# Kernel optimization log

Measured on AMD Instinct MI355X. Metric: run time of the kernel, lower is better.

Reference implementation:

```python
import jax, jax.numpy as jnp
import numpy as np

DIM = 1024
DEPTH = 4
D_STATE = 16
D_CONV = 4
D_INNER = 2 * DIM
DT_RANK = (DIM + 15) // 16  # 64, ceil(dim/16) as in mamba-ssm
B_SZ, L = 4, 2048


def setup_inputs() -> dict:
    key = jax.random.key(0)
    ks = jax.random.split(key, 10)
    s = 0.02
    x = jax.random.normal(ks[0], (B_SZ, L, DIM), jnp.float32)
    in_proj_w = jax.random.normal(ks[1], (DEPTH, 2 * D_INNER, DIM), jnp.float32) * s
    conv_w = jax.random.normal(ks[2], (DEPTH, D_INNER, D_CONV), jnp.float32) * 0.2
    conv_b = jnp.zeros((DEPTH, D_INNER), jnp.float32)
    x_proj_w = jax.random.normal(ks[3], (DEPTH, DT_RANK + 2 * D_STATE, D_INNER), jnp.float32) * s
    dt_proj_w = jax.random.normal(ks[4], (DEPTH, D_INNER, DT_RANK), jnp.float32) * s
    # bias init so softplus(bias) ~ 0.01 (mamba dt_init)
    dt_proj_b = jnp.full((DEPTH, D_INNER), float(np.log(np.expm1(0.01))), jnp.float32)
    # S4D-real init: A = -(1..d_state)
    A_log = jnp.broadcast_to(jnp.log(jnp.arange(1, D_STATE + 1, dtype=jnp.float32)), (D_INNER, D_STATE))
    A_log = jnp.broadcast_to(A_log, (DEPTH, D_INNER, D_STATE))
    D = jnp.ones((DEPTH, D_INNER), jnp.float32)
    out_proj_w = jax.random.normal(ks[5], (DEPTH, DIM, D_INNER), jnp.float32) * s
    return {"x": x, "in_proj_w": in_proj_w, "conv_w": conv_w, "conv_b": conv_b,
            "x_proj_w": x_proj_w, "dt_proj_w": dt_proj_w, "dt_proj_b": dt_proj_b,
            "A_log": A_log, "D": D, "out_proj_w": out_proj_w}


def _selective_scan(u, delta, A, Bm, Cm, D):
    # u, delta: [B, L, d_inner]; Bm, Cm: [B, L, d_state]; A: [d_inner, d_state]
    def step(h, inp):
        u_t, d_t, b_t, c_t = inp  # [B,di], [B,di], [B,ds], [B,ds]
        dA = jnp.exp(d_t[:, :, None] * A)                 # [B,di,ds]
        h = dA * h + (d_t * u_t)[:, :, None] * b_t[:, None, :]
        y = jnp.einsum('bds,bs->bd', h, c_t)
        return h, y

    h0 = jnp.zeros((u.shape[0], u.shape[2], A.shape[1]), u.dtype)
    xs = (u.transpose(1, 0, 2), delta.transpose(1, 0, 2),
          Bm.transpose(1, 0, 2), Cm.transpose(1, 0, 2))
    _, ys = jax.lax.scan(step, h0, xs)                     # ys: [L,B,di]
    return ys.transpose(1, 0, 2) + u * D


def _mamba_layer(x, in_w, cw, cb, xp_w, dtw, dtb, A_log, D, ow):
    xz = jnp.einsum('bld,ed->ble', x, in_w)               # [B,L,2*di]
    xi, z = jnp.split(xz, 2, axis=-1)
    # causal depthwise conv over L
    xc = jax.lax.conv_general_dilated(
        xi.transpose(0, 2, 1),                             # [B,di,L]
        cw[:, None, :],                                    # [di,1,k]
        window_strides=(1,), padding=[(D_CONV - 1, 0)],
        feature_group_count=D_INNER,
        dimension_numbers=('NCH', 'OIH', 'NCH'))
    xc = jax.nn.silu(xc.transpose(0, 2, 1) + cb)           # [B,L,di]
    dbc = jnp.einsum('bld,ed->ble', xc, xp_w)              # [B,L,dt_rank+2*ds]
    dt, Bm, Cm = jnp.split(dbc, [DT_RANK, DT_RANK + D_STATE], axis=-1)
    delta = jax.nn.softplus(jnp.einsum('blr,dr->bld', dt, dtw) + dtb)
    A = -jnp.exp(A_log)
    y = _selective_scan(xc, delta, A, Bm, Cm, D)
    y = y * jax.nn.silu(z)
    return jnp.einsum('bld,od->blo', y, ow)


def reference(x, in_proj_w, conv_w, conv_b, x_proj_w, dt_proj_w, dt_proj_b, A_log, D, out_proj_w):
    for i in range(DEPTH):
        x = _mamba_layer(x, in_proj_w[i], conv_w[i], conv_b[i], x_proj_w[i],
                         dt_proj_w[i], dt_proj_b[i], A_log[i], D[i], out_proj_w[i])
    return x
```

## Files before the change

kernel.cpp:

```cpp
#include <hip/hip_runtime.h>
#include <hip/hip_bf16.h>
#include <math.h>

#define DIMK 1024
#define NDEPTH 4
#define DS 16
#define DCONV 4
#define DI 2048
#define DTR 64
#define NB 4
#define SL 2048
#define MT (NB * SL)
#define NXZ (2 * DI)
#define NDBC (DTR + 2 * DS)

typedef float f32x4 __attribute__((ext_vector_type(4)));
typedef short short8 __attribute__((ext_vector_type(8)));
typedef short short4v __attribute__((ext_vector_type(4)));

__device__ inline unsigned short f2bf(float f) {
    unsigned u = __builtin_bit_cast(unsigned, f);
    unsigned r = (u + 0x7FFFu + ((u >> 16) & 1u)) >> 16;
    return (unsigned short)r;
}
__device__ inline float bf2f(unsigned short h) {
    unsigned u = ((unsigned)h) << 16;
    return __builtin_bit_cast(float, u);
}
__device__ inline void split_bf(float f, unsigned short& hi, unsigned short& lo) {
    hi = f2bf(f);
    lo = f2bf(f - bf2f(hi));
}
__device__ inline unsigned short cvt1(float f) {
    __hip_bfloat16 t = __float2bfloat16(f);
    return __builtin_bit_cast(unsigned short, t);
}
__device__ inline void mfma16(f32x4& d, short8 a, short8 b) {
    asm volatile("v_mfma_f32_16x16x32_bf16 %0, %1, %2, %0"
                 : "+v"(d) : "v"(a), "v"(b));
}
__device__ __forceinline__ float dpp_sum16(float p) {
    asm("v_add_f32_dpp %0, %0, %0 quad_perm:[1,0,3,2] row_mask:0xf bank_mask:0xf bound_ctrl:0" : "+v"(p));
    asm("v_add_f32_dpp %0, %0, %0 quad_perm:[2,3,0,1] row_mask:0xf bank_mask:0xf bound_ctrl:0" : "+v"(p));
    asm("v_add_f32_dpp %0, %0, %0 row_ror:4 row_mask:0xf bank_mask:0xf bound_ctrl:0" : "+v"(p));
    asm("v_add_f32_dpp %0, %0, %0 row_ror:8 row_mask:0xf bank_mask:0xf bound_ctrl:0" : "+v"(p));
    return p;
}
__device__ __forceinline__ float exp2_raw(float x) {
    float r;
    asm("v_exp_f32 %0, %1" : "=v"(r) : "v"(x));
    return r;
}
__device__ __forceinline__ void gload16(const unsigned short* g, unsigned short* l) {
    __builtin_amdgcn_global_load_lds(
        (const __attribute__((address_space(1))) unsigned int*)(g),
        (__attribute__((address_space(3))) unsigned int*)(l),
        16, 0, 0);
}

__global__ __launch_bounds__(256) void cvt_bf16(
    const float* __restrict__ s, unsigned short* __restrict__ d, int n4)
{
    const int g = blockIdx.x * 256 + threadIdx.x;
    if (g < n4) {
        const float4 f = *(const float4*)(s + (size_t)g * 4);
        short4v v;
        v[0] = (short)cvt1(f.x); v[1] = (short)cvt1(f.y);
        v[2] = (short)cvt1(f.z); v[3] = (short)cvt1(f.w);
        *(short4v*)(d + (size_t)g * 4) = v;
    }
}

__global__ __launch_bounds__(256) void cvt_layer(
    const float* __restrict__ wi, const float* __restrict__ owp,
    const float* __restrict__ dtwp,
    unsigned short* __restrict__ wi16, unsigned short* __restrict__ ow16,
    unsigned short* __restrict__ dtwh, unsigned short* __restrict__ dtwl,
    int fastd)
{
    int g = blockIdx.x * 256 + threadIdx.x;
    const int n4w = NXZ * DIMK / 4;
    const int n4o = DIMK * DI / 4;
    const int n4d = DI * DTR / 4;
    if (g < n4w) {
        const float4 f = *(const float4*)(wi + (size_t)g * 4);
        short4v v;
        v[0] = (short)cvt1(f.x); v[1] = (short)cvt1(f.y);
        v[2] = (short)cvt1(f.z); v[3] = (short)cvt1(f.w);
        *(short4v*)(wi16 + (size_t)g * 4) = v;
        return;
    }
    g -= n4w;
    if (g < n4o) {
        const float4 f = *(const float4*)(owp + (size_t)g * 4);
        short4v v;
        v[0] = (short)cvt1(f.x); v[1] = (short)cvt1(f.y);
        v[2] = (short)cvt1(f.z); v[3] = (short)cvt1(f.w);
        *(short4v*)(ow16 + (size_t)g * 4) = v;
        return;
    }
    g -= n4o;
    if (g < n4d && fastd) {
        const float4 f = *(const float4*)(dtwp + (size_t)g * 4);
        short4v h4, l4;
        #pragma unroll
        for (int e = 0; e < 4; ++e) {
            unsigned short h, l;
            split_bf((&f.x)[e], h, l);
            h4[e] = (short)h; l4[e] = (short)l;
        }
        *(short4v*)(dtwh + (size_t)g * 4) = h4;
        *(short4v*)(dtwl + (size_t)g * 4) = l4;
    }
}

template <int CBF>
__global__ __launch_bounds__(256) void gemm_bb(
    const unsigned short* __restrict__ A, const unsigned short* __restrict__ B,
    void* __restrict__ Cv, int K, int lda, int ldb, int ldc)
{
    __shared__ unsigned short As[2][128 * 32];
    __shared__ unsigned short Bs[2][128 * 32];
    int id = blockIdx.y * gridDim.x + blockIdx.x;
    const int qq = (gridDim.x * gridDim.y) >> 3;
    id = (id & 7) * qq + (id >> 3);
    const int bm = (id / gridDim.x) * 128, bn = (id % gridDim.x) * 128;

    const int tid = threadIdx.x;
    const int wv = tid >> 6, ln = tid & 63;
    const int wr = wv >> 1, wc = wv & 1;
    const int fr = ln & 15, kg = ln >> 4;
    const int sr0 = wv * 32 + (ln >> 2);
    const int sr1 = sr0 + 16;
    const int sl = ln & 3;
    const int cg0 = sl ^ ((sr0 >> 1) & 3);
    const int cg1 = sl ^ ((sr1 >> 1) & 3);
    const unsigned short* pa0 = A + (size_t)(bm + sr0) * lda + cg0 * 8;
    const unsigned short* pa1 = A + (size_t)(bm + sr1) * lda + cg1 * 8;
    const unsigned short* pb0 = B + (size_t)(bn + sr0) * ldb + cg0 * 8;
    const unsigned short* pb1 = B + (size_t)(bn + sr1) * ldb + cg1 * 8;
    const int ldst0 = (wv * 32 + 0) * 32;
    const int ldst1 = (wv * 32 + 16) * 32;
    int offA[4], offB[4];
    #pragma unroll
    for (int f = 0; f < 4; ++f) {
        const int ra = wr * 64 + f * 16 + fr;
        offA[f] = ra * 32 + ((kg ^ ((ra >> 1) & 3)) * 8);
        const int rb = wc * 64 + f * 16 + fr;
        offB[f] = rb * 32 + ((kg ^ ((rb >> 1) & 3)) * 8);
    }
    f32x4 acc[4][4] = {};
    gload16(pa0, &As[0][ldst0]);
    gload16(pa1, &As[0][ldst1]);
    gload16(pb0, &Bs[0][ldst0]);
    gload16(pb1, &Bs[0][ldst1]);
    __syncthreads();
    int cur = 0;
    for (int k0 = 0; k0 < K; k0 += 32) {
        const int nxt = cur ^ 1;
        if (k0 + 32 < K) {
            gload16(pa0 + k0 + 32, &As[nxt][ldst0]);
            gload16(pa1 + k0 + 32, &As[nxt][ldst1]);
            gload16(pb0 + k0 + 32, &Bs[nxt][ldst0]);
            gload16(pb1 + k0 + 32, &Bs[nxt][ldst1]);
        }
        short8 af[4], bw[4];
        #pragma unroll
        for (int f = 0; f < 4; ++f) {
            af[f] = *(const short8*)&As[cur][offA[f]];
            bw[f] = *(const short8*)&Bs[cur][offB[f]];
        }
        #pragma unroll
        for (int fi = 0; fi < 4; ++fi)
            #pragma unroll
            for (int fj = 0; fj < 4; ++fj)
                mfma16(acc[fi][fj], af[fi], bw[fj]);
        __syncthreads();
        cur = nxt;
    }
    #pragma unroll
    for (int fi = 0; fi < 4; ++fi) {
        const int m0 = bm + wr * 64 + fi * 16 + kg * 4;
        #pragma unroll
        for (int fj = 0; fj < 4; ++fj) {
            const int n = bn + wc * 64 + fj * 16 + fr;
            #pragma unroll
            for (int q = 0; q < 4; ++q) {
                if (CBF) {
                    unsigned short* Cs = (unsigned short*)Cv;
                    Cs[(size_t)(m0 + q) * ldc + n] = cvt1(acc[fi][fj][q]);
                } else {
                    float* Cf = (float*)Cv;
                    Cf[(size_t)(m0 + q) * ldc + n] = acc[fi][fj][q];
                }
            }
        }
    }
}

template <int CBF>
__global__ __launch_bounds__(256) void gemm_fb(
    const float* __restrict__ A, const unsigned short* __restrict__ B,
    void* __restrict__ Cv, int K, int lda, int ldb, int ldc)
{
    __shared__ unsigned short As[2][128 * 32];
    __shared__ unsigned short Bs[2][128 * 32];
    int id = blockIdx.y * gridDim.x + blockIdx.x;
    const int qq = (gridDim.x * gridDim.y) >> 3;
    id = (id & 7) * qq + (id >> 3);
    const int bm = (id / gridDim.x) * 128, bn = (id % gridDim.x) * 128;

    const int tid = threadIdx.x;
    const int wv = tid >> 6, ln = tid & 63;
    const int wr = wv >> 1, wc = wv & 1;
    const int fr = ln & 15, kg = ln >> 4;
    const int r = tid >> 1, hf = tid & 1;
    const int sr0 = wv * 32 + (ln >> 2);
    const int sr1 = sr0 + 16;
    const int sl = ln & 3;
    const int cg0 = sl ^ ((sr0 >> 1) & 3);
    const int cg1 = sl ^ ((sr1 >> 1) & 3);
    const unsigned short* pb0 = B + (size_t)(bn + sr0) * ldb + cg0 * 8;
    const unsigned short* pb1 = B + (size_t)(bn + sr1) * ldb + cg1 * 8;
    const int ldst0 = (wv * 32 + 0) * 32;
    const int ldst1 = (wv * 32 + 16) * 32;
    const float* ga = A + (size_t)(bm + r) * lda + hf * 16;
    const int pk0 = (2 * hf + 0) ^ ((r >> 1) & 3);
    const int pk1 = (2 * hf + 1) ^ ((r >> 1) & 3);
    int offA[4], offB[4];
    #pragma unroll
    for (int f = 0; f < 4; ++f) {
        const int ra = wr * 64 + f * 16 + fr;
        offA[f] = ra * 32 + ((kg ^ ((ra >> 1) & 3)) * 8);
        const int rb = wc * 64 + f * 16 + fr;
        offB[f] = rb * 32 + ((kg ^ ((rb >> 1) & 3)) * 8);
    }
    f32x4 acc[4][4] = {};
    {
        float4 f0 = *(const float4*)(ga + 0);
        float4 f1 = *(const float4*)(ga + 4);
        float4 f2 = *(const float4*)(ga + 8);
        float4 f3 = *(const float4*)(ga + 12);
        short8 v;
        v[0] = (short)cvt1(f0.x); v[1] = (short)cvt1(f0.y);
        v[2] = (short)cvt1(f0.z); v[3] = (short)cvt1(f0.w);
        v[4] = (short)cvt1(f1.x); v[5] = (short)cvt1(f1.y);
        v[6] = (short)cvt1(f1.z); v[7] = (short)cvt1(f1.w);
        *(short8*)&As[0][r * 32 + pk0 * 8] = v;
        v[0] = (short)cvt1(f2.x); v[1] = (short)cvt1(f2.y);
        v[2] = (short)cvt1(f2.z); v[3] = (short)cvt1(f2.w);
        v[4] = (short)cvt1(f3.x); v[5] = (short)cvt1(f3.y);
        v[6] = (short)cvt1(f3.z); v[7] = (short)cvt1(f3.w);
        *(short8*)&As[0][r * 32 + pk1 * 8] = v;
        gload16(pb0, &Bs[0][ldst0]);
        gload16(pb1, &Bs[0][ldst1]);
    }
    __syncthreads();
    int cur = 0;
    for (int k0 = 0; k0 < K; k0 += 32) {
        const int nxt = cur ^ 1;
        const bool more = (k0 + 32 < K);
        float4 f0, f1, f2, f3;
        if (more) {
            gload16(pb0 + k0 + 32, &Bs[nxt][ldst0]);
            gload16(pb1 + k0 + 32, &Bs[nxt][ldst1]);
            f0 = *(const float4*)(ga + k0 + 32);
            f1 = *(const float4*)(ga + k0 + 36);
            f2 = *(const float4*)(ga + k0 + 40);
            f3 = *(const float4*)(ga + k0 + 44);
        }
        short8 af[4], bw[4];
        #pragma unroll
        for (int f = 0; f < 4; ++f) {
            af[f] = *(const short8*)&As[cur][offA[f]];
            bw[f] = *(const short8*)&Bs[cur][offB[f]];
        }
        #pragma unroll
        for (int fi = 0; fi < 4; ++fi)
            #pragma unroll
            for (int fj = 0; fj < 4; ++fj)
                mfma16(acc[fi][fj], af[fi], bw[fj]);
        if (more) {
            short8 v;
            v[0] = (short)cvt1(f0.x); v[1] = (short)cvt1(f0.y);
            v[2] = (short)cvt1(f0.z); v[3] = (short)cvt1(f0.w);
            v[4] = (short)cvt1(f1.x); v[5] = (short)cvt1(f1.y);
            v[6] = (short)cvt1(f1.z); v[7] = (short)cvt1(f1.w);
            *(short8*)&As[nxt][r * 32 + pk0 * 8] = v;
            v[0] = (short)cvt1(f2.x); v[1] = (short)cvt1(f2.y);
            v[2] = (short)cvt1(f2.z); v[3] = (short)cvt1(f2.w);
            v[4] = (short)cvt1(f3.x); v[5] = (short)cvt1(f3.y);
            v[6] = (short)cvt1(f3.z); v[7] = (short)cvt1(f3.w);
            *(short8*)&As[nxt][r * 32 + pk1 * 8] = v;
        }
        __syncthreads();
        cur = nxt;
    }
    #pragma unroll
    for (int fi = 0; fi < 4; ++fi) {
        const int m0 = bm + wr * 64 + fi * 16 + kg * 4;
        #pragma unroll
        for (int fj = 0; fj < 4; ++fj) {
            const int n = bn + wc * 64 + fj * 16 + fr;
            #pragma unroll
            for (int q = 0; q < 4; ++q) {
                if (CBF) {
                    unsigned short* Cs = (unsigned short*)Cv;
                    Cs[(size_t)(m0 + q) * ldc + n] = cvt1(acc[fi][fj][q]);
                } else {
                    float* Cf = (float*)Cv;
                    Cf[(size_t)(m0 + q) * ldc + n] = acc[fi][fj][q];
                }
            }
        }
    }
}

__global__ __launch_bounds__(256) void gemm_mfma(
    const float* __restrict__ A, const float* __restrict__ W,
    float* __restrict__ C, int K, int lda, int ldc)
{
    __shared__ unsigned short As[128 * 32];
    __shared__ unsigned short Ws[128 * 32];
    const int tid = threadIdx.x;
    const int bm = blockIdx.y * 128;
    const int bn = blockIdx.x * 128;
    const int r = tid >> 1;
    const int h = tid & 1;
    const int wv = tid >> 6;
    const int wr = wv >> 1;
    const int wc = wv & 1;
    const int ln = tid & 63;
    const int fr = ln & 15;
    const int kg = ln >> 4;
    f32x4 acc[4][4] = {};
    const float* ga = A + (size_t)(bm + r) * lda + h * 16;
    const float* gw = W + (size_t)(bn + r) * K + h * 16;
    for (int k0 = 0; k0 < K; k0 += 32) {
        #pragma unroll
        for (int p = 0; p < 2; ++p) {
            const int pk = (2 * h + p) ^ ((r >> 1) & 3);
            float4 f0 = *(const float4*)(ga + k0 + p * 8);
            float4 f1 = *(const float4*)(ga + k0 + p * 8 + 4);
            short8 v;
            v[0] = (short)cvt1(f0.x); v[1] = (short)cvt1(f0.y);
            v[2] = (short)cvt1(f0.z); v[3] = (short)cvt1(f0.w);
            v[4] = (short)cvt1(f1.x); v[5] = (short)cvt1(f1.y);
            v[6] = (short)cvt1(f1.z); v[7] = (short)cvt1(f1.w);
            *(short8*)&As[r * 32 + pk * 8] = v;
            f0 = *(const float4*)(gw + k0 + p * 8);
            f1 = *(const float4*)(gw + k0 + p * 8 + 4);
            v[0] = (short)cvt1(f0.x); v[1] = (short)cvt1(f0.y);
            v[2] = (short)cvt1(f0.z); v[3] = (short)cvt1(f0.w);
            v[4] = (short)cvt1(f1.x); v[5] = (short)cvt1(f1.y);
            v[6] = (short)cvt1(f1.z); v[7] = (short)cvt1(f1.w);
            *(short8*)&Ws[r * 32 + pk * 8] = v;
        }
        __syncthreads();
        short8 af[4], bw[4];
        #pragma unroll
        for (int f = 0; f < 4; ++f) {
            const int ra = wr * 64 + f * 16 + fr;
            af[f] = *(const short8*)&As[ra * 32 + ((kg ^ ((ra >> 1) & 3)) * 8)];
            const int rb = wc * 64 + f * 16 + fr;
            bw[f] = *(const short8*)&Ws[rb * 32 + ((kg ^ ((rb >> 1) & 3)) * 8)];
        }
        #pragma unroll
        for (int fi = 0; fi < 4; ++fi)
            #pragma unroll
            for (int fj = 0; fj < 4; ++fj)
                mfma16(acc[fi][fj], af[fi], bw[fj]);
        __syncthreads();
    }
    #pragma unroll
    for (int fi = 0; fi < 4; ++fi) {
        const int m0 = bm + wr * 64 + fi * 16 + kg * 4;
        #pragma unroll
        for (int fj = 0; fj < 4; ++fj) {
            const int n = bn + wc * 64 + fj * 16 + fr;
            #pragma unroll
            for (int q = 0; q < 4; ++q)
                C[(size_t)(m0 + q) * ldc + n] = acc[fi][fj][q];
        }
    }
}

template <int WRDT>
__global__ __launch_bounds__(256) void gemm_xproj(
    const float* __restrict__ A, const float* __restrict__ W,
    float* __restrict__ C, int K, int lda,
    unsigned short* __restrict__ dth, unsigned short* __restrict__ dtl)
{
    __shared__ unsigned short Ah[128 * 32], Al[128 * 32];
    __shared__ unsigned short Wh[32 * 32], Wl[32 * 32];
    const int tid = threadIdx.x;
    const int bm = blockIdx.y * 128;
    const int bn = blockIdx.x * 32;
    const int r = tid >> 1, hf = tid & 1;
    const int wv = tid >> 6;
    const int ln = tid & 63, fr = ln & 15, kg = ln >> 4;
    const int wsr = tid >> 3;
    const int wc4 = (tid & 7) << 2;
    f32x4 acc[2][2] = {};
    const float* ga = A + (size_t)(bm + r) * lda + hf * 16;
    const float* gw = W + (size_t)(bn + wsr) * K + wc4;
    for (int k0 = 0; k0 < K; k0 += 32) {
        #pragma unroll
        for (int j = 0; j < 4; ++j) {
            const int col = hf * 16 + j * 4;
            const int ad = r * 32 + (((col >> 3) ^ ((r >> 1) & 3)) << 3) + (col & 7);
            const float4 fa = *(const float4*)(ga + k0 + j * 4);
            short4v h4, l4;
            #pragma unroll
            for (int e = 0; e < 4; ++e) {
                unsigned short hh, llo;
                split_bf((&fa.x)[e], hh, llo);
                h4[e] = (short)hh; l4[e] = (short)llo;
            }
            *(short4v*)&Ah[ad] = h4;
            *(short4v*)&Al[ad] = l4;
        }
        {
            const int ad = wsr * 32 + (((wc4 >> 3) ^ ((wsr >> 1) & 3)) << 3) + (wc4 & 7);
            const float4 fw = *(const float4*)(gw + k0);
            short4v h4, l4;
            #pragma unroll
            for (int e = 0; e < 4; ++e) {
                unsigned short hh, llo;
                split_bf((&fw.x)[e], hh, llo);
                h4[e] = (short)hh; l4[e] = (short)llo;
            }
            *(short4v*)&Wh[ad] = h4;
            *(short4v*)&Wl[ad] = l4;
        }
        __syncthreads();
        short8 ah[2], alo[2], bh[2], bl[2];
        #pragma unroll
        for (int f = 0; f < 2; ++f) {
            const int ra = wv * 32 + f * 16 + fr;
            const int ao = ra * 32 + ((kg ^ ((ra >> 1) & 3)) * 8);
            ah[f]  = *(const short8*)&Ah[ao];
            alo[f] = *(const short8*)&Al[ao];
            const int rb = f * 16 + fr;
            const int bo = rb * 32 + ((kg ^ ((rb >> 1) & 3)) * 8);
            bh[f] = *(const short8*)&Wh[bo];
            bl[f] = *(const short8*)&Wl[bo];
        }
        #pragma unroll
        for (int fi = 0; fi < 2; ++fi)
            #pragma unroll
            for (int fj = 0; fj < 2; ++fj) {
                mfma16(acc[fi][fj], ah[fi], bh[fj]);
                mfma16(acc[fi][fj], ah[fi], bl[fj]);
                mfma16(acc[fi][fj], alo[fi], bh[fj]);
            }
        __syncthreads();
    }
    #pragma unroll
    for (int fi = 0; fi < 2; ++fi) {
        const int m0 = bm + wv * 32 + fi * 16 + kg * 4;
        #pragma unroll
        for (int fj = 0; fj < 2; ++fj) {
            const int n = bn + fj * 16 + fr;
            #pragma unroll
            for (int q = 0; q < 4; ++q) {
                const float v = acc[fi][fj][q];
                C[(size_t)(m0 + q) * NDBC + n] = v;
                if (WRDT && n < DTR) {
                    unsigned short hh, llo;
                    split_bf(v, hh, llo);
                    dth[(size_t)(m0 + q) * DTR + n] = hh;
                    dtl[(size_t)(m0 + q) * DTR + n] = llo;
                }
            }
        }
    }
}

__global__ __launch_bounds__(256) void gemm_delta(
    const float* __restrict__ A, const float* __restrict__ W,
    float* __restrict__ C, const float* __restrict__ bias)
{
    __shared__ unsigned short Ah[128 * 32], Al[128 * 32];
    __shared__ unsigned short Wh[128 * 32], Wl[128 * 32];
    const int tid = threadIdx.x;
    const int bm = blockIdx.y * 128;
    const int bn = blockIdx.x * 128;
    const int r = tid >> 1, hf = tid & 1;
    const int wv = tid >> 6, wr = wv >> 1, wc = wv & 1;
    const int ln = tid & 63, fr = ln & 15, kg = ln >> 4;
    f32x4 acc[4][4] = {};
    const float* ga = A + (size_t)(bm + r) * NDBC + hf * 16;
    const float* gw = W + (size_t)(bn + r) * DTR + hf * 16;
    for (int k0 = 0; k0 < DTR; k0 += 32) {
        #pragma unroll
        for (int j = 0; j < 4; ++j) {
            const int col = hf * 16 + j * 4;
            const int ad = r * 32 + (((col >> 3) ^ ((r >> 1) & 3)) << 3) + (col & 7);
            const float4 fa = *(const float4*)(ga + k0 + j * 4);
            const float4 fw = *(const float4*)(gw + k0 + j * 4);
            short4v ah4, al4, wh4, wl4;
            #pragma unroll
            for (int e = 0; e < 4; ++e) {
                unsigned short hh, llo;
                split_bf((&fa.x)[e], hh, llo);
                ah4[e] = (short)hh; al4[e] = (short)llo;
                split_bf((&fw.x)[e], hh, llo);
                wh4[e] = (short)hh; wl4[e] = (short)llo;
            }
            *(short4v*)&Ah[ad] = ah4; *(short4v*)&Al[ad] = al4;
            *(short4v*)&Wh[ad] = wh4; *(short4v*)&Wl[ad] = wl4;
        }
        __syncthreads();
        short8 ah[4], alo[4], bh[4], bl[4];
        #pragma unroll
        for (int f = 0; f < 4; ++f) {
            const int ra = wr * 64 + f * 16 + fr;
            const int ao = ra * 32 + ((kg ^ ((ra >> 1) & 3)) * 8);
            ah[f]  = *(const short8*)&Ah[ao];
            alo[f] = *(const short8*)&Al[ao];
            const int rb = wc * 64 + f * 16 + fr;
            const int bo = rb * 32 + ((kg ^ ((rb >> 1) & 3)) * 8);
            bh[f] = *(const short8*)&Wh[bo];
            bl[f] = *(const short8*)&Wl[bo];
        }
        #pragma unroll
        for (int fi = 0; fi < 4; ++fi)
            #pragma unroll
            for (int fj = 0; fj < 4; ++fj) {
                mfma16(acc[fi][fj], ah[fi], bh[fj]);
                mfma16(acc[fi][fj], ah[fi], bl[fj]);
                mfma16(acc[fi][fj], alo[fi], bh[fj]);
            }
        __syncthreads();
    }
    #pragma unroll
    for (int fi = 0; fi < 4; ++fi) {
        const int m0 = bm + wr * 64 + fi * 16 + kg * 4;
        #pragma unroll
        for (int fj = 0; fj < 4; ++fj) {
            const int n = bn + wc * 64 + fj * 16 + fr;
            const float bb = bias[n];
            #pragma unroll
            for (int q = 0; q < 4; ++q) {
                float v = acc[fi][fj][q] + bb;
                v = (v > 20.f) ? v : log1pf(__expf(v));
                C[(size_t)(m0 + q) * NXZ + n] = v;
            }
        }
    }
}

__global__ __launch_bounds__(256) void gemm_delta_pre(
    const unsigned short* __restrict__ Ahg, const unsigned short* __restrict__ Alg,
    const unsigned short* __restrict__ Whg, const unsigned short* __restrict__ Wlg,
    float* __restrict__ C, const float* __restrict__ bias)
{
    __shared__ unsigned short sAh[128 * 64], sAl[128 * 64];
    __shared__ unsigned short sWh[128 * 64], sWl[128 * 64];
    const int tid = threadIdx.x;
    const int bm = blockIdx.y * 128;
    const int bn = blockIdx.x * 128;
    const int wv = tid >> 6, ln = tid & 63;
    const int wr = wv >> 1, wc = wv & 1;
    const int fr = ln & 15, kg = ln >> 4;
    const int srow = ln >> 3;
    const int g = ln & 7;
    const int half = g >> 2, sub = g & 3;
    #pragma unroll
    for (int j = 0; j < 4; ++j) {
        const int row = wv * 32 + j * 8 + srow;
        const int sub2 = sub ^ ((row >> 1) & 3);
        const int scol = half * 32 + sub2 * 8;
        const int dst = (wv * 32 + j * 8) * 64;
        gload16(Ahg + (size_t)(bm + row) * DTR + scol, sAh + dst);
        gload16(Alg + (size_t)(bm + row) * DTR + scol, sAl + dst);
        gload16(Whg + (size_t)(bn + row) * DTR + scol, sWh + dst);
        gload16(Wlg + (size_t)(bn + row) * DTR + scol, sWl + dst);
    }
    __syncthreads();
    f32x4 acc[4][4] = {};
    #pragma unroll
    for (int ks = 0; ks < 2; ++ks) {
        short8 ah[4], alo[4], bh[4], bl[4];
        #pragma unroll
        for (int f = 0; f < 4; ++f) {
            const int ra = wr * 64 + f * 16 + fr;
            const int ao = ra * 64 + ks * 32 + ((kg ^ ((ra >> 1) & 3)) * 8);
            ah[f]  = *(const short8*)&sAh[ao];
            alo[f] = *(const short8*)&sAl[ao];
            const int rb = wc * 64 + f * 16 + fr;
            const int bo = rb * 64 + ks * 32 + ((kg ^ ((rb >> 1) & 3)) * 8);
            bh[f] = *(const short8*)&sWh[bo];
            bl[f] = *(const short8*)&sWl[bo];
        }
        #pragma unroll
        for (int fi = 0; fi < 4; ++fi)
            #pragma unroll
            for (int fj = 0; fj < 4; ++fj) {
                mfma16(acc[fi][fj], ah[fi], bh[fj]);
                mfma16(acc[fi][fj], ah[fi], bl[fj]);
                mfma16(acc[fi][fj], alo[fi], bh[fj]);
            }
    }
    #pragma unroll
    for (int fi = 0; fi < 4; ++fi) {
        const int m0 = bm + wr * 64 + fi * 16 + kg * 4;
        #pragma unroll
        for (int fj = 0; fj < 4; ++fj) {
            const int n = bn + wc * 64 + fj * 16 + fr;
            const float bb = bias[n];
            #pragma unroll
            for (int q = 0; q < 4; ++q) {
                float v = acc[fi][fj][q] + bb;
                v = (v > 20.f) ? v : log1pf(__expf(v));
                C[(size_t)(m0 + q) * NXZ + n] = v;
            }
        }
    }
}

__global__ __launch_bounds__(256) void conv_silu(
    const float* __restrict__ xz, const float* __restrict__ cw,
    const float* __restrict__ cb, float* __restrict__ xc)
{
    const int g = blockIdx.x * 256 + threadIdx.x;
    const int c4 = g & (DI / 4 - 1);
    const int mq = g >> 9;
    const int m0 = mq << 2;
    const int l0 = m0 & (SL - 1);
    const int c = c4 << 2;
    const float4 w0 = *(const float4*)(cw + (size_t)(c + 0) * DCONV);
    const float4 w1 = *(const float4*)(cw + (size_t)(c + 1) * DCONV);
    const float4 w2 = *(const float4*)(cw + (size_t)(c + 2) * DCONV);
    const float4 w3 = *(const float4*)(cw + (size_t)(c + 3) * DCONV);
    const float4 cb4 = *(const float4*)(cb + c);
    float4 x[7];
    #pragma unroll
    for (int i = 0; i < 7; ++i) {
        if (l0 - 3 + i >= 0)
            x[i] = *(const float4*)(xz + (size_t)(m0 - 3 + i) * NXZ + c);
        else
            x[i] = make_float4(0.f, 0.f, 0.f, 0.f);
    }
    #pragma unroll
    for (int j = 0; j < 4; ++j) {
        float4 acc = cb4;
        #pragma unroll
        for (int k = 0; k < DCONV; ++k) {
            const float4 v = x[j + k];
            acc.x = fmaf(v.x, (&w0.x)[k], acc.x);
            acc.y = fmaf(v.y, (&w1.x)[k], acc.y);
            acc.z = fmaf(v.z, (&w2.x)[k], acc.z);
            acc.w = fmaf(v.w, (&w3.x)[k], acc.w);
        }
        acc.x = acc.x / (1.f + __expf(-acc.x));
        acc.y = acc.y / (1.f + __expf(-acc.y));
        acc.z = acc.z / (1.f + __expf(-acc.z));
        acc.w = acc.w / (1.f + __expf(-acc.w));
        *(float4*)(xc + (size_t)(m0 + j) * DI + c) = acc;
    }
}

template <int YBF>
__global__ __launch_bounds__(256) void scan_k(
    const float* u, const float* __restrict__ dbc,
    const float* __restrict__ xz, void* __restrict__ yv,
    const float* __restrict__ Alog, const float* __restrict__ Dl)
{
    const int b = blockIdx.y;
    const int c0 = blockIdx.x * 16;
    const int tid = threadIdx.x;
    const int ch = tid >> 4;
    const int s = tid & 15;
    const float Aa = -__expf(Alog[(size_t)(c0 + ch) * DS + s]) * 1.44269504088896f;
    __shared__ float sdl[16][68];
    __shared__ float sxb[16][68];
    __shared__ float sbc[32][68];
    __shared__ float sy[2][64][16];
    __shared__ float sD[16];
    if (tid < 16) sD[tid] = Dl[c0 + tid];
    __syncthreads();
    float h = 0.f;
    const int row = tid >> 2;
    const int q = (tid & 3) << 2;
    int pp = 0;
    for (int t0b = 0; t0b < SL; t0b += 64) {
        const size_t mb = (size_t)b * SL + t0b;
        const float4 dlv = *(const float4*)(xz + (mb + row) * NXZ + c0 + q);
        const float4 uv  = *(const float4*)(u  + (mb + row) * DI + c0 + q);
        const float4 zv  = *(const float4*)(xz + (mb + row) * NXZ + DI + c0 + q);
        float4 p0, p1;
        #pragma unroll
        for (int j = 0; j < 4; ++j) {
            const float dl = (&dlv.x)[j], uu = (&uv.x)[j], zz = (&zv.x)[j];
            const float w = zz / (1.f + __expf(-zz));
            sdl[q + j][row] = dl;
            sxb[q + j][row] = dl * uu;
            (&p1.x)[j] = w;
            (&p0.x)[j] = uu * sD[q + j] * w;
        }
        #pragma unroll
        for (int p = 0; p < 2; ++p) {
            const int idx = p * 256 + tid;
            const int r2 = idx >> 3, q2 = (idx & 7) << 2;
            const float4 v = *(const float4*)(dbc + (mb + r2) * NDBC + DTR + q2);
            sbc[q2 + 0][r2] = v.x; sbc[q2 + 1][r2] = v.y;
            sbc[q2 + 2][r2] = v.z; sbc[q2 + 3][r2] = v.w;
        }
        __syncthreads();
        for (int it = 0; it < 16; ++it) {
            const int t0 = it * 4;
            const float4 dl4 = *(const float4*)&sdl[ch][t0];
            const float4 xb4 = *(const float4*)&sxb[ch][t0];
            const float4 B4  = *(const float4*)&sbc[s][t0];
            const float4 C4  = *(const float4*)&sbc[16 + s][t0];
            float py0, py1, py2, py3;
            {
                const float dA = exp2_raw(dl4.x * Aa);
                h = fmaf(dA, h, xb4.x * B4.x);
                py0 = dpp_sum16(h * C4.x);
            }
            {
                const float dA = exp2_raw(dl4.y * Aa);
                h = fmaf(dA, h, xb4.y * B4.y);
                py1 = dpp_sum16(h * C4.y);
            }
            {
                const float dA = exp2_raw(dl4.z * Aa);
                h = fmaf(dA, h, xb4.z * B4.z);
                py2 = dpp_sum16(h * C4.z);
            }
            {
                const float dA = exp2_raw(dl4.w * Aa);
                h = fmaf(dA, h, xb4.w * B4.w);
                py3 = dpp_sum16(h * C4.w);
            }
            if (s < 4) {
                const int t = t0 + s;
                const float lo_ = (s & 1) ? py1 : py0;
                const float hi_ = (s & 1) ? py3 : py2;
                sy[pp][t][ch] = (s & 2) ? hi_ : lo_;
            }
        }
        __syncthreads();
        if (YBF) {
            unsigned short* y16 = (unsigned short*)yv;
            short4v s4;
            #pragma unroll
            for (int e = 0; e < 4; ++e)
                s4[e] = (short)cvt1(fmaf(sy[pp][row][q + e],
                                         (&p1.x)[e], (&p0.x)[e]));
            *(short4v*)(y16 + (mb + row) * DI + c0 + q) = s4;
        } else {
            float* y = (float*)yv;
            float4 yvv;
            #pragma unroll
            for (int e = 0; e < 4; ++e)
                (&yvv.x)[e] = fmaf(sy[pp][row][q + e], (&p1.x)[e], (&p0.x)[e]);
            *(float4*)(y + (mb + row) * DI + c0 + q) = yvv;
        }
        pp ^= 1;
    }
}

extern "C" void kernel_launch(void* const* d_in, const int* in_sizes, int n_in,
                              void* d_out, int out_size, void* d_ws, size_t ws_size,
                              hipStream_t stream)
{
    const float* x0   = (const float*)d_in[0];
    const float* in_w = (const float*)d_in[1];
    const float* cw   = (const float*)d_in[2];
    const float* cb   = (const float*)d_in[3];
    const float* xpw  = (const float*)d_in[4];
    const float* dtw  = (const float*)d_in[5];
    const float* dtb  = (const float*)d_in[6];
    const float* Alog = (const float*)d_in[7];
    const float* Dp   = (const float*)d_in[8];
    const float* ow   = (const float*)d_in[9];

    const size_t perB = (size_t)SL * (NXZ + DI + NDBC) * sizeof(float);
    const size_t wby  = ((size_t)NXZ * DIMK + (size_t)DIMK * DI) * 2;
    int nbc = 0, fast = 0;
    if (ws_size >= 4 * perB + wby)      { nbc = 4; fast = 1; }
    else if (ws_size >= 2 * perB + wby) { nbc = 2; fast = 1; }
    else if (ws_size >= perB + wby)     { nbc = 1; fast = 1; }
    else if (ws_size >= 4 * perB)       { nbc = 4; }
    else if (ws_size >= 2 * perB)       { nbc = 2; }
    else if (ws_size >= perB)           { nbc = 1; }
    else return;
    const int nchunks = NB / nbc;
    const int M = nbc * SL;
    const size_t dtby = ((size_t)DI * DTR * 2 + (size_t)M * DTR * 2) * 2;
    const size_t yby  = (size_t)M * DI * 2;
    const size_t base = (size_t)nbc * perB + wby;
    const int fastd = fast && (ws_size >= base + dtby);
    const int fasty = fastd && (ws_size >= base + dtby + yby);

    float* xz  = (float*)d_ws;
    float* xc  = xz + (size_t)M * NXZ;
    float* dbc = xc + (size_t)M * DI;
    unsigned short* wi16 = (unsigned short*)(dbc + (size_t)M * NDBC);
    unsigned short* ow16 = wi16 + (size_t)NXZ * DIMK;
    unsigned short* dtwh = ow16 + (size_t)DIMK * DI;
    unsigned short* dtwl = dtwh + (size_t)DI * DTR;
    unsigned short* dth  = dtwl + (size_t)DI * DTR;
    unsigned short* dtl  = dth + (size_t)M * DTR;
    unsigned short* y16  = dtl + (size_t)M * DTR;

    unsigned short* xb16 = (unsigned short*)d_out + (size_t)MT * DIMK;
    float* xbuf = (float*)d_out;

    const dim3 blk(256);
    const int ncv = (NXZ * DIMK / 4) + (DIMK * DI / 4) + (DI * DTR / 4);
    for (int ly = 0; ly < NDEPTH; ++ly) {
        const float* Wi   = in_w + (size_t)ly * NXZ * DIMK;
        const float* cwl  = cw   + (size_t)ly * DI * DCONV;
        const float* cbl  = cb   + (size_t)ly * DI;
        const float* xpl  = xpw  + (size_t)ly * NDBC * DI;
        const float* dtwl_ = dtw + (size_t)ly * DI * DTR;
        const float* dtbl = dtb  + (size_t)ly * DI;
        const float* Al   = Alog + (size_t)ly * DI * DS;
        const float* Dl   = Dp   + (size_t)ly * DI;
        const float* owl  = ow   + (size_t)ly * DIMK * DI;

        if (fast)
            cvt_layer<<<dim3((ncv + 255) / 256), blk, 0, stream>>>(
                Wi, owl, dtwl_, wi16, ow16, dtwh, dtwl, fastd);

        for (int ck = 0; ck < nchunks; ++ck) {
            if (fast) {
                if (ly == 0) {
                    const float* xin = x0 + (size_t)ck * M * DIMK;
                    gemm_fb<0><<<dim3(NXZ / 128, M / 128), blk, 0, stream>>>(
                        xin, wi16, xz, DIMK, DIMK, DIMK, NXZ);
                } else {
                    const unsigned short* xin16 = xb16 + (size_t)ck * M * DIMK;
                    gemm_bb<0><<<dim3(NXZ / 128, M / 128), blk, 0, stream>>>(
                        xin16, wi16, xz, DIMK, DIMK, DIMK, NXZ);
                }
                conv_silu<<<dim3(M * (DI / 16) / 256), blk, 0, stream>>>(
                    xz, cwl, cbl, xc);
            } else {
                const float* xin = (ly == 0 ? x0 : xbuf) + (size_t)ck * M * DIMK;
                gemm_mfma<<<dim3(NXZ / 128, M / 128), blk, 0, stream>>>(
                    xin, Wi, xz, DIMK, DIMK, NXZ);
                conv_silu<<<dim3(M * (DI / 16) / 256), blk, 0, stream>>>(
                    xz, cwl, cbl, xc);
            }
            if (fastd) {
                gemm_xproj<1><<<dim3(3, M / 128), blk, 0, stream>>>(
                    xc, xpl, dbc, DI, DI, dth, dtl);
                gemm_delta_pre<<<dim3(DI / 128, M / 128), blk, 0, stream>>>(
                    dth, dtl, dtwh, dtwl, xz, dtbl);
            } else {
                gemm_xproj<0><<<dim3(3, M / 128), blk, 0, stream>>>(
                    xc, xpl, dbc, DI, DI, nullptr, nullptr);
                gemm_delta<<<dim3(DI / 128, M / 128), blk, 0, stream>>>(
                    dbc, dtwl_, xz, dtbl);
            }
            if (fasty) {
                scan_k<1><<<dim3(DI / 16, nbc), blk, 0, stream>>>(
                    xc, dbc, xz, y16, Al, Dl);
            } else {
                scan_k<0><<<dim3(DI / 16, nbc), blk, 0, stream>>>(
                    xc, dbc, xz, xc, Al, Dl);
            }
            if (fast) {
                void* dst = (ly < NDEPTH - 1)
                    ? (void*)(xb16 + (size_t)ck * M * DIMK)
                    : (void*)((float*)d_out + (size_t)ck * M * DIMK);
                if (fasty) {
                    if (ly < NDEPTH - 1)
                        gemm_bb<1><<<dim3(DIMK / 128, M / 128), blk, 0, stream>>>(
                            y16, ow16, dst, DI, DI, DI, DIMK);
                    else
                        gemm_bb<0><<<dim3(DIMK / 128, M / 128), blk, 0, stream>>>(
                            y16, ow16, dst, DI, DI, DI, DIMK);
                } else {
                    if (ly < NDEPTH - 1)
                        gemm_fb<1><<<dim3(DIMK / 128, M / 128), blk, 0, stream>>>(
                            xc, ow16, dst, DI, DI, DI, DIMK);
                    else
                        gemm_fb<0><<<dim3(DIMK / 128, M / 128), blk, 0, stream>>>(
                            xc, ow16, dst, DI, DI, DI, DIMK);
                }
            } else {
                float* xdst = (ly == NDEPTH - 1 ? (float*)d_out : xbuf) +
                              (size_t)ck * M * DIMK;
                gemm_mfma<<<dim3(DIMK / 128, M / 128), blk, 0, stream>>>(
                    xc, owl, xdst, DI, DI, DIMK);
            }
        }
    }
}
```

Before: 1.921 ms.

## Split conv output into bf16 hi/lo pairs and use MFMA x_proj on pre-split operands

Adds a fastx path. The conv+SiLU kernel now writes its output as bf16 high/low pairs, and x_proj weights are split once per layer. A new double-buffered x_proj GEMM consumes these pairs directly with three MFMA products, and the scan reconstructs u from the pair. Layer 0's input is converted to bf16 up front so every layer uses the bf16 in_proj GEMM. The aim is to remove the per-tile fp32-to-bf16 splitting inside the old x_proj GEMM and to reduce fp32 traffic. The cost is extra workspace, the requirement that the workspace is large enough, and a slight precision change on layer 0's input.

```diff
diff --git a/kernel.cpp b/kernel.cpp
--- a/kernel.cpp
+++ b/kernel.cpp
@@ -73,15 +73,17 @@
 
 __global__ __launch_bounds__(256) void cvt_layer(
     const float* __restrict__ wi, const float* __restrict__ owp,
-    const float* __restrict__ dtwp,
+    const float* __restrict__ dtwp, const float* __restrict__ xpwp,
     unsigned short* __restrict__ wi16, unsigned short* __restrict__ ow16,
     unsigned short* __restrict__ dtwh, unsigned short* __restrict__ dtwl,
-    int fastd)
+    unsigned short* __restrict__ xpwh, unsigned short* __restrict__ xpwl,
+    int fastd, int fastx)
 {
     int g = blockIdx.x * 256 + threadIdx.x;
     const int n4w = NXZ * DIMK / 4;
     const int n4o = DIMK * DI / 4;
     const int n4d = DI * DTR / 4;
+    const int n4x = NDBC * DI / 4;
     if (g < n4w) {
         const float4 f = *(const float4*)(wi + (size_t)g * 4);
         short4v v;
@@ -100,8 +102,24 @@
         return;
     }
     g -= n4o;
-    if (g < n4d && fastd) {
-        const float4 f = *(const float4*)(dtwp + (size_t)g * 4);
+    if (g < n4d) {
+        if (fastd) {
+            const float4 f = *(const float4*)(dtwp + (size_t)g * 4);
+            short4v h4, l4;
+            #pragma unroll
+            for (int e = 0; e < 4; ++e) {
+                unsigned short h, l;
+                split_bf((&f.x)[e], h, l);
+                h4[e] = (short)h; l4[e] = (short)l;
+            }
+            *(short4v*)(dtwh + (size_t)g * 4) = h4;
+            *(short4v*)(dtwl + (size_t)g * 4) = l4;
+        }
+        return;
+    }
+    g -= n4d;
+    if (g < n4x && fastx) {
+        const float4 f = *(const float4*)(xpwp + (size_t)g * 4);
         short4v h4, l4;
         #pragma unroll
         for (int e = 0; e < 4; ++e) {
@@ -109,8 +127,8 @@
             split_bf((&f.x)[e], h, l);
             h4[e] = (short)h; l4[e] = (short)l;
         }
-        *(short4v*)(dtwh + (size_t)g * 4) = h4;
-        *(short4v*)(dtwl + (size_t)g * 4) = l4;
+        *(short4v*)(xpwh + (size_t)g * 4) = h4;
+        *(short4v*)(xpwl + (size_t)g * 4) = l4;
     }
 }
 
@@ -385,6 +403,106 @@
     }
 }
 
+__global__ __launch_bounds__(256) void gemm_xproj_pre(
+    const unsigned short* __restrict__ Ahg, const unsigned short* __restrict__ Alg,
+    const unsigned short* __restrict__ Whg, const unsigned short* __restrict__ Wlg,
+    float* __restrict__ C,
+    unsigned short* __restrict__ dth, unsigned short* __restrict__ dtl)
+{
+    __shared__ unsigned short Ahs[2][128 * 32], Als[2][128 * 32];
+    __shared__ unsigned short Whs[2][32 * 32], Wls[2][32 * 32];
+    int id = blockIdx.y * gridDim.x + blockIdx.x;
+    const int qq = (gridDim.x * gridDim.y) >> 3;
+    id = (id & 7) * qq + (id >> 3);
+    const int bm = (id / gridDim.x) * 128, bn = (id % gridDim.x) * 32;
+
+    const int tid = threadIdx.x;
+    const int wv = tid >> 6, ln = tid & 63;
+    const int fr = ln & 15, kg = ln >> 4;
+    const int sr0 = wv * 32 + (ln >> 2);
+    const int sr1 = sr0 + 16;
+    const int sl = ln & 3;
+    const int cg0 = sl ^ ((sr0 >> 1) & 3);
+    const int cg1 = sl ^ ((sr1 >> 1) & 3);
+    const unsigned short* pah0 = Ahg + (size_t)(bm + sr0) * DI + cg0 * 8;
+    const unsigned short* pah1 = Ahg + (size_t)(bm + sr1) * DI + cg1 * 8;
+    const unsigned short* pal0 = Alg + (size_t)(bm + sr0) * DI + cg0 * 8;
+    const unsigned short* pal1 = Alg + (size_t)(bm + sr1) * DI + cg1 * 8;
+    const int lA0 = (wv * 32 + 0) * 32;
+    const int lA1 = (wv * 32 + 16) * 32;
+    const int wrow = (wv & 1) * 16 + (ln >> 2);
+    const int cgw = sl ^ ((wrow >> 1) & 3);
+    const unsigned short* pw = ((wv < 2) ? Whg : Wlg) + (size_t)(bn + wrow) * DI + cgw * 8;
+    const int lW = ((wv & 1) * 16) * 32;
+    unsigned short* wdst[2];
+    wdst[0] = (wv < 2) ? &Whs[0][lW] : &Wls[0][lW];
+    wdst[1] = (wv < 2) ? &Whs[1][lW] : &Wls[1][lW];
+
+    int offA[2], offW[2];
+    #pragma unroll
+    for (int f = 0; f < 2; ++f) {
+        const int ra = wv * 32 + f * 16 + fr;
+        offA[f] = ra * 32 + ((kg ^ ((ra >> 1) & 3)) * 8);
+        const int rb = f * 16 + fr;
+        offW[f] = rb * 32 + ((kg ^ ((rb >> 1) & 3)) * 8);
+    }
+    f32x4 acc[2][2] = {};
+    gload16(pah0, &Ahs[0][lA0]);
+    gload16(pah1, &Ahs[0][lA1]);
+    gload16(pal0, &Als[0][lA0]);
+    gload16(pal1, &Als[0][lA1]);
+    gload16(pw, wdst[0]);
+    __syncthreads();
+    int cur = 0;
+    for (int k0 = 0; k0 < DI; k0 += 32) {
+        const int nxt = cur ^ 1;
+        if (k0 + 32 < DI) {
+            gload16(pah0 + k0 + 32, &Ahs[nxt][lA0]);
+            gload16(pah1 + k0 + 32, &Ahs[nxt][lA1]);
+            gload16(pal0 + k0 + 32, &Als[nxt][lA0]);
+            gload16(pal1 + k0 + 32, &Als[nxt][lA1]);
+            gload16(pw + k0 + 32, wdst[nxt]);
+        }
+        short8 ah[2], alo[2], bh[2], bl[2];
+        #pragma unroll
+        for (int f = 0; f < 2; ++f) {
+            ah[f]  = *(const short8*)&Ahs[cur][offA[f]];
+            alo[f] = *(const short8*)&Als[cur][offA[f]];
+            bh[f]  = *(const short8*)&Whs[cur][offW[f]];
+            bl[f]  = *(const short8*)&Wls[cur][offW[f]];
+        }
+        #pragma unroll
+        for (int fi = 0; fi < 2; ++fi)
+            #pragma unroll
+            for (int fj = 0; fj < 2; ++fj) {
+                mfma16(acc[fi][fj], ah[fi], bh[fj]);
+                mfma16(acc[fi][fj], ah[fi], bl[fj]);
+                mfma16(acc[fi][fj], alo[fi], bh[fj]);
+            }
+        __syncthreads();
+        cur = nxt;
+    }
+    #pragma unroll
+    for (int fi = 0; fi < 2; ++fi) {
+        const int m0 = bm + wv * 32 + fi * 16 + kg * 4;
+        #pragma unroll
+        for (int fj = 0; fj < 2; ++fj) {
+            const int n = bn + fj * 16 + fr;
+            #pragma unroll
+            for (int q = 0; q < 4; ++q) {
+                const float v = acc[fi][fj][q];
+                C[(size_t)(m0 + q) * NDBC + n] = v;
+                if (n < DTR) {
+                    unsigned short hh, llo;
+                    split_bf(v, hh, llo);
+                    dth[(size_t)(m0 + q) * DTR + n] = hh;
+                    dtl[(size_t)(m0 + q) * DTR + n] = llo;
+                }
+            }
+        }
+    }
+}
+
 template <int WRDT>
 __global__ __launch_bounds__(256) void gemm_xproj(
     const float* __restrict__ A, const float* __restrict__ W,
@@ -662,9 +780,60 @@
     }
 }
 
-template <int YBF>
+__global__ __launch_bounds__(256) void conv_silu_split(
+    const float* __restrict__ xz, const float* __restrict__ cw,
+    const float* __restrict__ cb, unsigned short* __restrict__ xch,
+    unsigned short* __restrict__ xcl)
+{
+    const int g = blockIdx.x * 256 + threadIdx.x;
+    const int c4 = g & (DI / 4 - 1);
+    const int mq = g >> 9;
+    const int m0 = mq << 2;
+    const int l0 = m0 & (SL - 1);
+    const int c = c4 << 2;
+    const float4 w0 = *(const float4*)(cw + (size_t)(c + 0) * DCONV);
+    const float4 w1 = *(const float4*)(cw + (size_t)(c + 1) * DCONV);
+    const float4 w2 = *(const float4*)(cw + (size_t)(c + 2) * DCONV);
+    const float4 w3 = *(const float4*)(cw + (size_t)(c + 3) * DCONV);
+    const float4 cb4 = *(const float4*)(cb + c);
+    float4 x[7];
+    #pragma unroll
+    for (int i = 0; i < 7; ++i) {
+        if (l0 - 3 + i >= 0)
+            x[i] = *(const float4*)(xz + (size_t)(m0 - 3 + i) * NXZ + c);
+        else
+            x[i] = make_float4(0.f, 0.f, 0.f, 0.f);
+    }
+    #pragma unroll
+    for (int j = 0; j < 4; ++j) {
+        float4 acc = cb4;
+        #pragma unroll
+        for (int k = 0; k < DCONV; ++k) {
+            const float4 v = x[j + k];
+            acc.x = fmaf(v.x, (&w0.x)[k], acc.x);
+            acc.y = fmaf(v.y, (&w1.x)[k], acc.y);
+            acc.z = fmaf(v.z, (&w2.x)[k], acc.z);
+            acc.w = fmaf(v.w, (&w3.x)[k], acc.w);
+        }
+        short4v h4, l4;
+        #pragma unroll
+        for (int e = 0; e < 4; ++e) {
+            float a = (&acc.x)[e];
+            a = a / (1.f + __expf(-a));
+            unsigned short hh, llo;
+            split_bf(a, hh, llo);
+            h4[e] = (short)hh; l4[e] = (short)llo;
+        }
+        *(short4v*)(xch + (size_t)(m0 + j) * DI + c) = h4;
+        *(short4v*)(xcl + (size_t)(m0 + j) * DI + c) = l4;
+    }
+}
+
+template <int YBF, int UBF>
 __global__ __launch_bounds__(256) void scan_k(
-    const float* u, const float* __restrict__ dbc,
+    const float* uf, const unsigned short* __restrict__ uh,
+    const unsigned short* __restrict__ ul,
+    const float* __restrict__ dbc,
     const float* __restrict__ xz, void* __restrict__ yv,
     const float* __restrict__ Alog, const float* __restrict__ Dl)
 {
@@ -688,8 +857,18 @@
     for (int t0b = 0; t0b < SL; t0b += 64) {
         const size_t mb = (size_t)b * SL + t0b;
         const float4 dlv = *(const float4*)(xz + (mb + row) * NXZ + c0 + q);
-        const float4 uv  = *(const float4*)(u  + (mb + row) * DI + c0 + q);
-        const float4 zv  = *(const float4*)(xz + (mb + row) * NXZ + DI + c0 + q);
+        float4 uv;
+        if (UBF) {
+            const short4v uh4 = *(const short4v*)(uh + (mb + row) * DI + c0 + q);
+            const short4v ul4 = *(const short4v*)(ul + (mb + row) * DI + c0 + q);
+            #pragma unroll
+            for (int e = 0; e < 4; ++e)
+                (&uv.x)[e] = bf2f((unsigned short)uh4[e]) +
+                             bf2f((unsigned short)ul4[e]);
+        } else {
+            uv = *(const float4*)(uf + (mb + row) * DI + c0 + q);
+        }
+        const float4 zv = *(const float4*)(xz + (mb + row) * NXZ + DI + c0 + q);
         float4 p0, p1;
         #pragma unroll
         for (int j = 0; j < 4; ++j) {
@@ -793,13 +972,17 @@
     const int M = nbc * SL;
     const size_t dtby = ((size_t)DI * DTR * 2 + (size_t)M * DTR * 2) * 2;
     const size_t yby  = (size_t)M * DI * 2;
+    const size_t xpby = (size_t)NDBC * DI * 2 * 2;
     const size_t base = (size_t)nbc * perB + wby;
     const int fastd = fast && (ws_size >= base + dtby);
     const int fasty = fastd && (ws_size >= base + dtby + yby);
+    const int fastx = fasty && (ws_size >= base + dtby + yby + xpby);
 
     float* xz  = (float*)d_ws;
     float* xc  = xz + (size_t)M * NXZ;
     float* dbc = xc + (size_t)M * DI;
+    unsigned short* xch = (unsigned short*)xc;
+    unsigned short* xcl = xch + (size_t)M * DI;
     unsigned short* wi16 = (unsigned short*)(dbc + (size_t)M * NDBC);
     unsigned short* ow16 = wi16 + (size_t)NXZ * DIMK;
     unsigned short* dtwh = ow16 + (size_t)DIMK * DI;
@@ -807,12 +990,19 @@
     unsigned short* dth  = dtwl + (size_t)DI * DTR;
     unsigned short* dtl  = dth + (size_t)M * DTR;
     unsigned short* y16  = dtl + (size_t)M * DTR;
+    unsigned short* xpwh = y16 + (size_t)M * DI;
+    unsigned short* xpwl = xpwh + (size_t)NDBC * DI;
 
     unsigned short* xb16 = (unsigned short*)d_out + (size_t)MT * DIMK;
     float* xbuf = (float*)d_out;
 
     const dim3 blk(256);
-    const int ncv = (NXZ * DIMK / 4) + (DIMK * DI / 4) + (DI * DTR / 4);
+    if (fastx) {
+        const int n4x = MT * DIMK / 4;
+        cvt_bf16<<<dim3(n4x / 256), blk, 0, stream>>>(x0, xb16, n4x);
+    }
+    const int ncv = (NXZ * DIMK / 4) + (DIMK * DI / 4) + (DI * DTR / 4) +
+                    (NDBC * DI / 4);
     for (int ly = 0; ly < NDEPTH; ++ly) {
         const float* Wi   = in_w + (size_t)ly * NXZ * DIMK;
         const float* cwl  = cw   + (size_t)ly * DI * DCONV;
@@ -826,10 +1016,32 @@
 
         if (fast)
             cvt_layer<<<dim3((ncv + 255) / 256), blk, 0, stream>>>(
-                Wi, owl, dtwl_, wi16, ow16, dtwh, dtwl, fastd);
+                Wi, owl, dtwl_, xpl, wi16, ow16, dtwh, dtwl, xpwh, xpwl,
+                fastd, fastx);
 
         for (int ck = 0; ck < nchunks; ++ck) {
-            if (fast) {
+            if (fastx) {
+                const unsigned short* xin16 = xb16 + (size_t)ck * M * DIMK;
+                gemm_bb<0><<<dim3(NXZ / 128, M / 128), blk, 0, stream>>>(
+                    xin16, wi16, xz, DIMK, DIMK, DIMK, NXZ);
+                conv_silu_split<<<dim3(M * (DI / 16) / 256), blk, 0, stream>>>(
+                    xz, cwl, cbl, xch, xcl);
+                gemm_xproj_pre<<<dim3(3, M / 128), blk, 0, stream>>>(
+                    xch, xcl, xpwh, xpwl, dbc, dth, dtl);
+                gemm_delta_pre<<<dim3(DI / 128, M / 128), blk, 0, stream>>>(
+                    dth, dtl, dtwh, dtwl, xz, dtbl);
+                scan_k<1, 1><<<dim3(DI / 16, nbc), blk, 0, stream>>>(
+                    nullptr, xch, xcl, dbc, xz, y16, Al, Dl);
+                void* dst = (ly < NDEPTH - 1)
+                    ? (void*)(xb16 + (size_t)ck * M * DIMK)
+                    : (void*)((float*)d_out + (size_t)ck * M * DIMK);
+                if (ly < NDEPTH - 1)
+                    gemm_bb<1><<<dim3(DIMK / 128, M / 128), blk, 0, stream>>>(
+                        y16, ow16, dst, DI, DI, DI, DIMK);
+                else
+                    gemm_bb<0><<<dim3(DIMK / 128, M / 128), blk, 0, stream>>>(
+                        y16, ow16, dst, DI, DI, DI, DIMK);
+            } else if (fast) {
                 if (ly == 0) {
                     const float* xin = x0 + (size_t)ck * M * DIMK;
                     gemm_fb<0><<<dim3(NXZ / 128, M / 128), blk, 0, stream>>>(
@@ -841,36 +1053,23 @@
                 }
                 conv_silu<<<dim3(M * (DI / 16) / 256), blk, 0, stream>>>(
                     xz, cwl, cbl, xc);
-            } else {
-                const float* xin = (ly == 0 ? x0 : xbuf) + (size_t)ck * M * DIMK;
-                gemm_mfma<<<dim3(NXZ / 128, M / 128), blk, 0, stream>>>(
-                    xin, Wi, xz, DIMK, DIMK, NXZ);
-                conv_silu<<<dim3(M * (DI / 16) / 256), blk, 0, stream>>>(
-                    xz, cwl, cbl, xc);
-            }
-            if (fastd) {
-                gemm_xproj<1><<<dim3(3, M / 128), blk, 0, stream>>>(
-                    xc, xpl, dbc, DI, DI, dth, dtl);
-                gemm_delta_pre<<<dim3(DI / 128, M / 128), blk, 0, stream>>>(
-                    dth, dtl, dtwh, dtwl, xz, dtbl);
-            } else {
-                gemm_xproj<0><<<dim3(3, M / 128), blk, 0, stream>>>(
-                    xc, xpl, dbc, DI, DI, nullptr, nullptr);
-                gemm_delta<<<dim3(DI / 128, M / 128), blk, 0, stream>>>(
-                    dbc, dtwl_, xz, dtbl);
-            }
-            if (fasty) {
-                scan_k<1><<<dim3(DI / 16, nbc), blk, 0, stream>>>(
-                    xc, dbc, xz, y16, Al, Dl);
-            } else {
-                scan_k<0><<<dim3(DI / 16, nbc), blk, 0, stream>>>(
-                    xc, dbc, xz, xc, Al, Dl);
-            }
-            if (fast) {
+                if (fastd) {
+                    gemm_xproj<1><<<dim3(3, M / 128), blk, 0, stream>>>(
+                        xc, xpl, dbc, DI, DI, dth, dtl);
+                    gemm_delta_pre<<<dim3(DI / 128, M / 128), blk, 0, stream>>>(
+                        dth, dtl, dtwh, dtwl, xz, dtbl);
+                } else {
+                    gemm_xproj<0><<<dim3(3, M / 128), blk, 0, stream>>>(
+                        xc, xpl, dbc, DI, DI, nullptr, nullptr);
+                    gemm_delta<<<dim3(DI / 128, M / 128), blk, 0, stream>>>(
+                        dbc, dtwl_, xz, dtbl);
+                }
                 void* dst = (ly < NDEPTH - 1)
                     ? (void*)(xb16 + (size_t)ck * M * DIMK)
                     : (void*)((float*)d_out + (size_t)ck * M * DIMK);
                 if (fasty) {
+                    scan_k<1, 0><<<dim3(DI / 16, nbc), blk, 0, stream>>>(
+                        xc, nullptr, nullptr, dbc, xz, y16, Al, Dl);
                     if (ly < NDEPTH - 1)
                         gemm_bb<1><<<dim3(DIMK / 128, M / 128), blk, 0, stream>>>(
                             y16, ow16, dst, DI, DI, DI, DIMK);
@@ -878,6 +1077,8 @@
                         gemm_bb<0><<<dim3(DIMK / 128, M / 128), blk, 0, stream>>>(
                             y16, ow16, dst, DI, DI, DI, DIMK);
                 } else {
+                    scan_k<0, 0><<<dim3(DI / 16, nbc), blk, 0, stream>>>(
+                        xc, nullptr, nullptr, dbc, xz, xc, Al, Dl);
                     if (ly < NDEPTH - 1)
                         gemm_fb<1><<<dim3(DIMK / 128, M / 128), blk, 0, stream>>>(
                             xc, ow16, dst, DI, DI, DI, DIMK);
@@ -886,6 +1087,17 @@
                             xc, ow16, dst, DI, DI, DI, DIMK);
                 }
             } else {
+                const float* xin = (ly == 0 ? x0 : xbuf) + (size_t)ck * M * DIMK;
+                gemm_mfma<<<dim3(NXZ / 128, M / 128), blk, 0, stream>>>(
+                    xin, Wi, xz, DIMK, DIMK, NXZ);
+                conv_silu<<<dim3(M * (DI / 16) / 256), blk, 0, stream>>>(
+                    xz, cwl, cbl, xc);
+                gemm_xproj<0><<<dim3(3, M / 128), blk, 0, stream>>>(
+                    xc, xpl, dbc, DI, DI, nullptr, nullptr);
+                gemm_delta<<<dim3(DI / 128, M / 128), blk, 0, stream>>>(
+                    dbc, dtwl_, xz, dtbl);
+                scan_k<0, 0><<<dim3(DI / 16, nbc), blk, 0, stream>>>(
+                    xc, nullptr, nullptr, dbc, xz, xc, Al, Dl);
                 float* xdst = (ly == NDEPTH - 1 ? (float*)d_out : xbuf) +
                               (size_t)ck * M * DIMK;
                 gemm_mfma<<<dim3(DIMK / 128, M / 128), blk, 0, stream>>>(
```

After: 1.650 ms. 1.16x faster.
